# Performance work log

Hardware: AMD Instinct MI355X
Metric: run time of the kernel (lower is better)

Reference implementation:

```python
import jax, jax.numpy as jnp
import numpy as np

B, S, E, H = 4, 1024, 1024, 16
D = E // H
LN_EPS = 1e-5
W_SCALE = 0.02  # keep pre-softmax scores positive and moderate


def _linear(x, W, b):
    return x @ W + b


def _layernorm(x, g, b):
    m = jnp.mean(x, axis=-1, keepdims=True)
    v = jnp.mean((x - m) ** 2, axis=-1, keepdims=True)
    return (x - m) * jax.lax.rsqrt(v + LN_EPS) * g + b


def setup_inputs() -> dict:
    key = jax.random.key(0)
    ks = jax.random.split(key, 24)
    u = lambda k, shape, s=1.0: jax.random.uniform(k, shape, dtype=jnp.float32) * s
    inp = {
        'value': u(ks[0], (B, S, E)),
        'key':   u(ks[1], (B, S, E)),
        'query': u(ks[2], (B, S, E)),
        'mask':  jnp.ones((B, 1, 1, S), dtype=jnp.int32),
        # attention projections (W stored as [in, out])
        'Wv': u(ks[3], (E, E), W_SCALE), 'bv': u(ks[4], (E,), W_SCALE),
        'Wk': u(ks[5], (E, E), W_SCALE), 'bk': u(ks[6], (E,), W_SCALE),
        'Wq': u(ks[7], (E, E), W_SCALE), 'bq': u(ks[8], (E,), W_SCALE),
        'Wo': u(ks[9], (E, E), W_SCALE), 'bo': u(ks[10], (E,), W_SCALE),
        # feed-forward
        'W1': u(ks[11], (E, 4 * E), W_SCALE), 'b1': u(ks[12], (4 * E,), W_SCALE),
        'W2': u(ks[13], (4 * E, E), W_SCALE), 'b2': u(ks[14], (E,), W_SCALE),
        # layer norms
        'g1': jnp.ones((E,), jnp.float32), 'be1': jnp.zeros((E,), jnp.float32),
        'g2': jnp.ones((E,), jnp.float32), 'be2': jnp.zeros((E,), jnp.float32),
    }
    return inp


def reference(value, key, query, mask, Wv, bv, Wk, bk, Wq, bq, Wo, bo,
              W1, b1, W2, b2, g1, be1, g2, be2):
    b, q_len, _ = query.shape
    v = _linear(value, Wv, bv).reshape(b, -1, H, D)   # [B,K,H,D]
    k = _linear(key, Wk, bk).reshape(b, -1, H, D)     # [B,K,H,D]
    q = _linear(query, Wq, bq).reshape(b, q_len, H, D)
    att = jnp.einsum('bqhd,bkhd->bhqk', q, k)         # raw scores
    att = jnp.where(mask == 0, -jnp.inf, att)
    att = jnp.power(att, -0.5)                        # custom score^{-1/2} transform
    att = jax.nn.softmax(att, axis=3)
    ctx = jnp.einsum('bhqk,bkhd->bqhd', att, v).reshape(b, q_len, E)
    attn_out = _linear(ctx, Wo, bo)
    x = _layernorm(attn_out + query, g1, be1)         # dropout = identity (eval)
    ff = _linear(jax.nn.relu(_linear(x, W1, b1)), W2, b2)
    return _layernorm(ff + x, g2, be2)
```

## Files before the change

kernel.cpp:

```cpp
#include <hip/hip_runtime.h>
#include <hip/hip_bf16.h>
#include <cstdint>

typedef __hip_bfloat16 bf16;
typedef float f32x4 __attribute__((ext_vector_type(4)));
typedef short bf16x8 __attribute__((ext_vector_type(8)));
typedef short bf16x4v __attribute__((ext_vector_type(4)));

#define S_LEN 1024
#define EDIM  1024

__device__ __forceinline__ float bfs2f(short s) {
  return __uint_as_float(((unsigned)(unsigned short)s) << 16);
}
__device__ __forceinline__ short f2bfs(float f) {
  union { __hip_bfloat16 h; short s; } u;
  u.h = __float2bfloat16(f);
  return u.s;
}
__device__ __forceinline__ void glds16(const void* g, void* l) {
  __builtin_amdgcn_global_load_lds(
      (const __attribute__((address_space(1))) void*)g,
      (__attribute__((address_space(3))) void*)l, 16, 0, 0);
}
__device__ __forceinline__ float score_xform(float s) {
  float r, e;
  asm("v_rsq_f32 %0, %1" : "=v"(r) : "v"(s));
  r *= 1.44269504088896f;
  asm("v_exp_f32 %0, %1" : "=v"(e) : "v"(r));
  return e;
}
__device__ __forceinline__ int xcd_swz(int bid, int nwg) {
  const int q = nwg >> 3, r = nwg & 7, xcd = bid & 7, j = bid >> 3;
  return (xcd < r ? xcd * (q + 1) : r * (q + 1) + (xcd - r) * q) + j;
}
#define BAR() do { __builtin_amdgcn_s_barrier(); asm volatile("" ::: "memory"); } while (0)
#define WAITV(n) asm volatile("s_waitcnt vmcnt(" #n ")" ::: "memory")

struct Prep { const float* win[6]; bf16* wout[6]; const float* ain[3]; bf16* aout[3]; };
__global__ __launch_bounds__(256)
void k_prep(Prep p) {
  const int t = blockIdx.x;
  const int tid = threadIdx.x;
  if (t < 1536) {
    int z, tr, tc, R, C;
    if (t < 512)       { z = t >> 7;  R = 1024; C = 1024; int i = t & 127;  tr = i >> 4; tc = i & 15; }
    else if (t < 1024) { z = 4; R = 1024; C = 4096; int i = t - 512;  tr = i >> 6; tc = i & 63; }
    else               { z = 5; R = 4096; C = 1024; int i = t - 1024; tr = i >> 4; tc = i & 15; }
    const float* in = p.win[z];
    bf16* out = p.wout[z];
    const int r0 = tr * 128, c0 = tc * 64;
    __shared__ bf16 tlds[64][130];
    const int rr = tid >> 4;
    const int cq = (tid & 15) * 4;
    float4 v[8];
#pragma unroll
    for (int pass = 0; pass < 8; pass++)
      v[pass] = *(const float4*)(in + (size_t)(r0 + pass * 16 + rr) * C + c0 + cq);
#pragma unroll
    for (int pass = 0; pass < 8; pass++) {
      const int r = pass * 16 + rr;
      tlds[cq + 0][r] = __float2bfloat16(v[pass].x);
      tlds[cq + 1][r] = __float2bfloat16(v[pass].y);
      tlds[cq + 2][r] = __float2bfloat16(v[pass].z);
      tlds[cq + 3][r] = __float2bfloat16(v[pass].w);
    }
    __syncthreads();
    const int e8 = (tid & 15) * 8;
    bf16x8 w[4];
#pragma unroll
    for (int pass = 0; pass < 4; pass++)
      w[pass] = *(const bf16x8*)(&tlds[pass * 16 + rr][e8]);
#pragma unroll
    for (int pass = 0; pass < 4; pass++)
      *(bf16x8*)(out + (size_t)(c0 + pass * 16 + rr) * R + r0 + e8) = w[pass];
  } else {
    const int idx = t - 1536;
    const int z = idx >> 8, chunk = idx & 255;
    const float4* in = (const float4*)p.ain[z];
    bf16x4v* out = (bf16x4v*)p.aout[z];
#pragma unroll
    for (int g = 0; g < 2; g++) {
      float4 v[8];
#pragma unroll
      for (int s = 0; s < 8; s++)
        v[s] = in[chunk * 4096 + (g * 8 + s) * 256 + tid];
#pragma unroll
      for (int s = 0; s < 8; s++) {
        bf16x4v o;
        o[0] = f2bfs(v[s].x); o[1] = f2bfs(v[s].y);
        o[2] = f2bfs(v[s].z); o[3] = f2bfs(v[s].w);
        out[chunk * 4096 + (g * 8 + s) * 256 + tid] = o;
      }
    }
  }
}

__global__ void k_transpose_v(const bf16* __restrict__ v, bf16* __restrict__ vt) {
  __shared__ bf16 t[32][33];
  const int bh = blockIdx.z;
  const bf16* in = v + (size_t)(bh >> 4) * S_LEN * EDIM + (bh & 15) * 64;
  bf16* out = vt + (size_t)bh * 64 * S_LEN;
  const int d0 = blockIdx.x * 32, s0 = blockIdx.y * 32;
  const int x = threadIdx.x;
  for (int yy = threadIdx.y; yy < 32; yy += 8)
    t[yy][x] = in[(size_t)(s0 + yy) * EDIM + d0 + x];
  __syncthreads();
  for (int yy = threadIdx.y; yy < 32; yy += 8)
    out[(size_t)(d0 + yy) * S_LEN + s0 + x] = t[x][yy];
}

template <int RELU, int OUT_F32, int HAS_BIAS>
__device__ __forceinline__ void gemm8_body(
    const bf16* __restrict__ A, int lda, const bf16* __restrict__ Bt, int ldb,
    const float* __restrict__ bias, void* __restrict__ Cout, int ldc,
    int K, int koff, int bm, int bn, char* smem) {
  const int tid = threadIdx.x, lane = tid & 63, wid = tid >> 6;
  const int wm = wid >> 2;
  const int wn = wid & 3;
  const int fr = lane & 15, fg = lane >> 4;
  const int sw = (fr & 7) << 4;

  const int rr = lane >> 3;
  const int cc = ((lane & 7) ^ rr) << 3;

  #define STG(src, ld, dstoff)                                                  \
    {                                                                           \
      const bf16* _s = (src);                                                   \
      _Pragma("unroll")                                                         \
      for (int _j = 0; _j < 2; _j++) {                                          \
        const int _L = wid * 2 + _j;                                            \
        glds16(_s + (size_t)(_L * 8 + rr) * (ld) + cc, smem + (dstoff) + _L * 1024); \
      }                                                                         \
    }

  const bf16* Abase = A + (size_t)bm * lda + koff;
  const bf16* Bbase = Bt + (size_t)bn * ldb + koff;
  const int nt = K >> 6;

  STG(Abase, lda, 0);
  STG(Abase + (size_t)128 * lda, lda, 16384);
  STG(Bbase, ldb, 98304);
  STG(Bbase + (size_t)128 * ldb, ldb, 98304 + 16384);
  STG(Abase + 64, lda, 32768);
  STG(Abase + (size_t)128 * lda + 64, lda, 32768 + 16384);
  STG(Bbase + 64, ldb, 131072);
  STG(Bbase + (size_t)128 * ldb + 64, ldb, 131072 + 16384);
  WAITV(8);
  BAR();

  f32x4 acc[8][4] = {};
  bf16x8 af[8][2], bfr[4][2];

  const int aRd = wm * 16384 + fr * 128;
  const int bRd = (wn >> 1) * 16384 + (wn & 1) * 8192 + fr * 128;
  const int c0s = (fg * 16) ^ sw;
  const int c1s = (64 + fg * 16) ^ sw;

  int sa = 0, sb = 0;
  for (int n = 0; n < nt; n++) {
    const char* pa = smem + sa * 32768;
    const char* pb = smem + 98304 + sb * 32768;
    const int kn = (n + 2) << 6;
    const bool st = (n + 2) < nt;
    const int sa2 = (sa >= 1) ? sa - 1 : 2;

#pragma unroll
    for (int j = 0; j < 4; j++) {
      bfr[j][0] = *(const bf16x8*)(pb + bRd + j * 2048 + c0s);
      bfr[j][1] = *(const bf16x8*)(pb + bRd + j * 2048 + c1s);
    }
#pragma unroll
    for (int i = 0; i < 8; i++) {
      af[i][0] = *(const bf16x8*)(pa + aRd + i * 2048 + c0s);
      af[i][1] = *(const bf16x8*)(pa + aRd + i * 2048 + c1s);
    }
    if (st) {
      STG(Abase + kn, lda, sa2 * 32768);
      STG(Abase + (size_t)128 * lda + kn, lda, sa2 * 32768 + 16384);
    }
    BAR();
    __builtin_amdgcn_s_setprio(1);
#pragma unroll
    for (int i = 0; i < 4; i++)
#pragma unroll
      for (int j = 0; j < 4; j++) {
        acc[i][j] = __builtin_amdgcn_mfma_f32_16x16x32_bf16(af[i][0], bfr[j][0], acc[i][j], 0, 0, 0);
        acc[i][j] = __builtin_amdgcn_mfma_f32_16x16x32_bf16(af[i][1], bfr[j][1], acc[i][j], 0, 0, 0);
      }
    __builtin_amdgcn_s_setprio(0);

    if (st) {
      STG(Bbase + kn, ldb, 98304 + sb * 32768);
      STG(Bbase + (size_t)128 * ldb + kn, ldb, 98304 + sb * 32768 + 16384);
    }
    __builtin_amdgcn_s_setprio(1);
#pragma unroll
    for (int i = 0; i < 4; i++)
#pragma unroll
      for (int j = 0; j < 4; j++) {
        acc[i + 4][j] = __builtin_amdgcn_mfma_f32_16x16x32_bf16(af[i + 4][0], bfr[j][0], acc[i + 4][j], 0, 0, 0);
        acc[i + 4][j] = __builtin_amdgcn_mfma_f32_16x16x32_bf16(af[i + 4][1], bfr[j][1], acc[i + 4][j], 0, 0, 0);
      }
    __builtin_amdgcn_s_setprio(0);
    if (st) { WAITV(8); } else { WAITV(0); }
    BAR();
    sa = (sa == 2) ? 0 : sa + 1;
    sb ^= 1;
  }
  #undef STG

  float bv4[4];
#pragma unroll
  for (int j = 0; j < 4; j++)
    bv4[j] = HAS_BIAS ? bias[bn + wn * 64 + j * 16 + fr] : 0.f;
#pragma unroll
  for (int i = 0; i < 8; i++) {
    const size_t rowb = (size_t)bm + wm * 128 + i * 16 + fg * 4;
#pragma unroll
    for (int r = 0; r < 4; r++) {
#pragma unroll
      for (int j = 0; j < 4; j++) {
        float v = acc[i][j][r] + bv4[j];
        if (RELU) v = fmaxf(v, 0.f);
        const size_t idx = (rowb + r) * (size_t)ldc + bn + wn * 64 + j * 16 + fr;
        if (OUT_F32) ((float*)Cout)[idx] = v;
        else ((bf16*)Cout)[idx] = __float2bfloat16(v);
      }
    }
  }
}

struct G8Args {
  const bf16* A; int lda; const bf16* Bt; int ldb; const float* bias;
  void* C[4]; int ldc; int koffz[4]; int Kzz[4];
};
template <int RELU, int OUT_F32, int HAS_BIAS>
__global__ __launch_bounds__(512, 2)
void k_gemm8(G8Args a) {
  __shared__ __align__(16) char smem[163840];
  const int nwg = gridDim.x * gridDim.y;
  const int bid = xcd_swz(blockIdx.y * gridDim.x + blockIdx.x, nwg);
  const int bx = bid % gridDim.x, by = bid / gridDim.x;
  const int z = blockIdx.z;
  gemm8_body<RELU, OUT_F32, HAS_BIAS>(
      a.A, a.lda, a.Bt, a.ldb, a.bias, a.C[z], a.ldc,
      a.Kzz[z], a.koffz[z], by * 256, bx * 256, smem);
}

struct QkvArgs { const bf16* A[3]; const bf16* B[3]; const float* bias[3]; bf16* C[3]; };
__global__ __launch_bounds__(512, 2)
void k_gemm8_qkv(QkvArgs p) {
  __shared__ __align__(16) char smem[163840];
  const int nwg = gridDim.x * gridDim.y;
  const int bid = xcd_swz(blockIdx.y * gridDim.x + blockIdx.x, nwg);
  const int bx = bid % (int)gridDim.x;
  int by = bid / (int)gridDim.x;
  const int grp = by >> 4;
  by &= 15;
  gemm8_body<0, 0, 1>(p.A[grp], 1024, p.B[grp], 1024, p.bias[grp],
                      (void*)p.C[grp], 1024, 1024, 0, by * 256, bx * 256, smem);
}

__global__ __launch_bounds__(256)
void k_attn(const bf16* __restrict__ q, const bf16* __restrict__ k,
            const bf16* __restrict__ vt, bf16* __restrict__ ctx) {
  const int bh = blockIdx.x;
  const int qt = blockIdx.y;
  const int b = bh >> 4, h = bh & 15;
  const int tid = threadIdx.x, lane = tid & 63, w = tid >> 6;
  const int fr = lane & 15, fg = lane >> 4;
  const bf16* Q  = q  + (size_t)b * S_LEN * EDIM + h * 64;
  const bf16* Kp = k  + (size_t)b * S_LEN * EDIM + h * 64;
  const bf16* V  = vt + (size_t)bh * 64 * S_LEN;

  __shared__ __align__(16) bf16 lK[2][64 * 64];
  __shared__ __align__(16) bf16 lV[2][64 * 64];
  __shared__ __align__(16) bf16 eL[4][32][72];

  const int srow = lane >> 3;
  const int scol = (((lane & 7) ^ srow) << 3);
  const int rsw  = (fr & 7) << 3;

  bf16x8 qf[2][2];
#pragma unroll
  for (int i = 0; i < 2; i++)
#pragma unroll
    for (int ks = 0; ks < 2; ks++)
      qf[i][ks] = *(const bf16x8*)(Q + (size_t)(qt * 128 + w * 32 + i * 16 + fr) * EDIM + ks * 32 + fg * 8);

#pragma unroll
  for (int c = 0; c < 2; c++) {
    const int r = w * 8 + c * 32 + srow;
    glds16(Kp + (size_t)r * EDIM + scol, (char*)&lK[0][(w * 8 + c * 32) * 64]);
    glds16(V + (size_t)r * S_LEN + scol, (char*)&lV[0][(w * 8 + c * 32) * 64]);
  }
  __syncthreads();

  f32x4 accO[2][4] = {};
  float lsum[2][4] = {};
  int cur = 0;
  for (int kt = 0; kt < S_LEN; kt += 64) {
    if (kt + 64 < S_LEN) {
#pragma unroll
      for (int c = 0; c < 2; c++) {
        const int r = w * 8 + c * 32 + srow;
        glds16(Kp + (size_t)(kt + 64 + r) * EDIM + scol,
               (char*)&lK[cur ^ 1][(w * 8 + c * 32) * 64]);
        glds16(V + (size_t)r * S_LEN + kt + 64 + scol,
               (char*)&lV[cur ^ 1][(w * 8 + c * 32) * 64]);
      }
    }
    f32x4 accS[2][4] = {};
#pragma unroll
    for (int ks = 0; ks < 2; ks++)
#pragma unroll
      for (int j = 0; j < 4; j++) {
        bf16x8 kf = *(const bf16x8*)(&lK[cur][(j * 16 + fr) * 64 + ((ks * 32 + fg * 8) ^ rsw)]);
#pragma unroll
        for (int i = 0; i < 2; i++)
          accS[i][j] = __builtin_amdgcn_mfma_f32_16x16x32_bf16(qf[i][ks], kf, accS[i][j], 0, 0, 0);
      }
#pragma unroll
    for (int i = 0; i < 2; i++)
#pragma unroll
      for (int j = 0; j < 4; j++)
#pragma unroll
        for (int r = 0; r < 4; r++) {
          float p = score_xform(accS[i][j][r]);
          lsum[i][r] += p;
          eL[w][i * 16 + fg * 4 + r][j * 16 + fr] = __float2bfloat16(p);
        }
#pragma unroll
    for (int ks = 0; ks < 2; ks++) {
      bf16x8 af[2];
#pragma unroll
      for (int i = 0; i < 2; i++)
        af[i] = *(const bf16x8*)(&eL[w][i * 16 + fr][ks * 32 + fg * 8]);
#pragma unroll
      for (int j = 0; j < 4; j++) {
        bf16x8 vf = *(const bf16x8*)(&lV[cur][(j * 16 + fr) * 64 + ((ks * 32 + fg * 8) ^ rsw)]);
#pragma unroll
        for (int i = 0; i < 2; i++)
          accO[i][j] = __builtin_amdgcn_mfma_f32_16x16x32_bf16(af[i], vf, accO[i][j], 0, 0, 0);
      }
    }
    __syncthreads();
    cur ^= 1;
  }

#pragma unroll
  for (int i = 0; i < 2; i++)
#pragma unroll
    for (int r = 0; r < 4; r++) {
      float s = lsum[i][r];
      s += __shfl_xor(s, 1, 64);
      s += __shfl_xor(s, 2, 64);
      s += __shfl_xor(s, 4, 64);
      s += __shfl_xor(s, 8, 64);
      lsum[i][r] = s;
    }
#pragma unroll
  for (int i = 0; i < 2; i++)
#pragma unroll
    for (int r = 0; r < 4; r++) {
      const size_t qrow = (size_t)qt * 128 + w * 32 + i * 16 + fg * 4 + r;
      const float inv = 1.0f / lsum[i][r];
#pragma unroll
      for (int j = 0; j < 4; j++)
        ctx[((size_t)b * S_LEN + qrow) * EDIM + h * 64 + j * 16 + fr] =
            __float2bfloat16(accO[i][j][r] * inv);
    }
}

struct LnP { const void* p[4]; };
template <int NP, int P_BF16, int RES_F32, int OUT_F32>
__global__ __launch_bounds__(256)
void k_ln_resN(LnP pp, const float* __restrict__ bias, const void* res_,
               const float* __restrict__ g, const float* __restrict__ be,
               void* out_) {
  const int row = blockIdx.x;
  const int tid = threadIdx.x;
  const int lane = tid & 63, wid = tid >> 6;
  const size_t base = (size_t)row * EDIM + tid * 4;
  float4 c = *(const float4*)(bias + tid * 4);
  float x[4] = {c.x, c.y, c.z, c.w};
#pragma unroll
  for (int t = 0; t < NP; t++) {
    if (P_BF16) {
      bf16x4v v = *(const bf16x4v*)((const bf16*)pp.p[t] + base);
#pragma unroll
      for (int i = 0; i < 4; i++) x[i] += bfs2f(v[i]);
    } else {
      float4 v = *(const float4*)((const float*)pp.p[t] + base);
      x[0] += v.x; x[1] += v.y; x[2] += v.z; x[3] += v.w;
    }
  }
  if (RES_F32) {
    float4 v = *(const float4*)((const float*)res_ + base);
    x[0] += v.x; x[1] += v.y; x[2] += v.z; x[3] += v.w;
  } else {
    bf16x4v v = *(const bf16x4v*)((const bf16*)res_ + base);
#pragma unroll
    for (int i = 0; i < 4; i++) x[i] += bfs2f(v[i]);
  }

  float s = x[0] + x[1] + x[2] + x[3];
#pragma unroll
  for (int o = 32; o >= 1; o >>= 1) s += __shfl_xor(s, o, 64);
  __shared__ float red[4], red2[4];
  if (lane == 0) red[wid] = s;
  __syncthreads();
  const float mean = (red[0] + red[1] + red[2] + red[3]) * (1.0f / 1024.0f);

  float d[4], s2 = 0.f;
#pragma unroll
  for (int i = 0; i < 4; i++) { d[i] = x[i] - mean; s2 += d[i] * d[i]; }
#pragma unroll
  for (int o = 32; o >= 1; o >>= 1) s2 += __shfl_xor(s2, o, 64);
  if (lane == 0) red2[wid] = s2;
  __syncthreads();
  const float var = (red2[0] + red2[1] + red2[2] + red2[3]) * (1.0f / 1024.0f);
  const float inv = rsqrtf(var + 1e-5f);

  float4 g4 = *(const float4*)(g + tid * 4);
  float4 b4 = *(const float4*)(be + tid * 4);
  float o0 = d[0] * inv * g4.x + b4.x;
  float o1 = d[1] * inv * g4.y + b4.y;
  float o2 = d[2] * inv * g4.z + b4.z;
  float o3 = d[3] * inv * g4.w + b4.w;
  if (OUT_F32) {
    *(float4*)((float*)out_ + base) = make_float4(o0, o1, o2, o3);
  } else {
    bf16x4v o;
    o[0] = f2bfs(o0); o[1] = f2bfs(o1); o[2] = f2bfs(o2); o[3] = f2bfs(o3);
    *(bf16x4v*)((bf16*)out_ + base) = o;
  }
}

extern "C" void kernel_launch(void* const* d_in, const int* in_sizes, int n_in,
                              void* d_out, int out_size, void* d_ws, size_t ws_size,
                              hipStream_t stream) {
  const float* value = (const float*)d_in[0];
  const float* key_  = (const float*)d_in[1];
  const float* query = (const float*)d_in[2];
  const float* Wv = (const float*)d_in[4];  const float* bv = (const float*)d_in[5];
  const float* Wk = (const float*)d_in[6];  const float* bk = (const float*)d_in[7];
  const float* Wq = (const float*)d_in[8];  const float* bq = (const float*)d_in[9];
  const float* Wo = (const float*)d_in[10]; const float* bo = (const float*)d_in[11];
  const float* W1 = (const float*)d_in[12]; const float* b1 = (const float*)d_in[13];
  const float* W2 = (const float*)d_in[14]; const float* b2 = (const float*)d_in[15];
  const float* g1 = (const float*)d_in[16]; const float* be1 = (const float*)d_in[17];
  const float* g2 = (const float*)d_in[18]; const float* be2 = (const float*)d_in[19];

  char* wsb = (char*)d_ws;
  const size_t MB = 1024 * 1024;
  bf16* W1T = (bf16*)(wsb + 0 * MB);
  bf16* W2T = (bf16*)(wsb + 8 * MB);
  bf16* WqT = (bf16*)(wsb + 16 * MB);
  bf16* WkT = (bf16*)(wsb + 18 * MB);
  bf16* WvT = (bf16*)(wsb + 20 * MB);
  bf16* WoT = (bf16*)(wsb + 22 * MB);
  bf16* qx  = (bf16*)(wsb + 24 * MB);
  bf16* kx  = (bf16*)(wsb + 32 * MB);
  bf16* vx  = (bf16*)(wsb + 40 * MB);
  bf16* qb  = (bf16*)(wsb + 48 * MB);
  bf16* kb  = (bf16*)(wsb + 56 * MB);
  bf16* vb  = (bf16*)(wsb + 64 * MB);
  bf16* vtb = (bf16*)(wsb + 72 * MB);
  bf16* ctx = (bf16*)(wsb + 24 * MB);
  float* p0w = (float*)(wsb + 32 * MB);
  float* p1w = (float*)(wsb + 48 * MB);
  float* p2w = (float*)(wsb + 64 * MB);
  bf16* xb  = (bf16*)(wsb + 16 * MB);
  bf16* h1  = (bf16*)(wsb + 24 * MB);
  bf16* fp0 = (bf16*)(wsb + 56 * MB);
  bf16* fp1 = (bf16*)(wsb + 64 * MB);
  bf16* fp2 = (bf16*)(wsb + 72 * MB);
  bf16* fp3 = (bf16*)(wsb + 80 * MB);

  const dim3 tb(32, 8);
  Prep pp;
  pp.win[0] = Wq; pp.wout[0] = WqT;
  pp.win[1] = Wk; pp.wout[1] = WkT;
  pp.win[2] = Wv; pp.wout[2] = WvT;
  pp.win[3] = Wo; pp.wout[3] = WoT;
  pp.win[4] = W1; pp.wout[4] = W1T;
  pp.win[5] = W2; pp.wout[5] = W2T;
  pp.ain[0] = query; pp.aout[0] = qx;
  pp.ain[1] = key_;  pp.aout[1] = kx;
  pp.ain[2] = value; pp.aout[2] = vx;
  k_prep<<<2304, 256, 0, stream>>>(pp);

  QkvArgs qp;
  qp.A[0] = qx; qp.B[0] = WqT; qp.bias[0] = bq; qp.C[0] = qb;
  qp.A[1] = kx; qp.B[1] = WkT; qp.bias[1] = bk; qp.C[1] = kb;
  qp.A[2] = vx; qp.B[2] = WvT; qp.bias[2] = bv; qp.C[2] = vb;
  k_gemm8_qkv<<<dim3(4, 48), 512, 0, stream>>>(qp);

  k_transpose_v<<<dim3(2, 32, 64), tb, 0, stream>>>(vb, vtb);
  k_attn<<<dim3(64, 8), 256, 0, stream>>>(qb, kb, vtb, ctx);

  G8Args wo;
  wo.A = ctx; wo.lda = 1024; wo.Bt = WoT; wo.ldb = 1024; wo.bias = nullptr;
  wo.C[0] = p0w; wo.C[1] = p1w; wo.C[2] = p2w; wo.C[3] = nullptr;
  wo.ldc = 1024;
  wo.koffz[0] = 0;   wo.Kzz[0] = 384;
  wo.koffz[1] = 384; wo.Kzz[1] = 320;
  wo.koffz[2] = 704; wo.Kzz[2] = 320;
  wo.koffz[3] = 0;   wo.Kzz[3] = 64;
  k_gemm8<0, 1, 0><<<dim3(4, 16, 3), 512, 0, stream>>>(wo);
  LnP l1; l1.p[0] = p0w; l1.p[1] = p1w; l1.p[2] = p2w; l1.p[3] = nullptr;
  k_ln_resN<3, 0, 1, 0><<<4096, 256, 0, stream>>>(l1, bo, query, g1, be1, xb);

  G8Args ff1;
  ff1.A = xb; ff1.lda = 1024; ff1.Bt = W1T; ff1.ldb = 1024; ff1.bias = b1;
  ff1.C[0] = h1; ff1.C[1] = nullptr; ff1.C[2] = nullptr; ff1.C[3] = nullptr;
  ff1.ldc = 4096;
  ff1.koffz[0] = 0; ff1.Kzz[0] = 1024;
  ff1.koffz[1] = 0; ff1.Kzz[1] = 64;
  ff1.koffz[2] = 0; ff1.Kzz[2] = 64;
  ff1.koffz[3] = 0; ff1.Kzz[3] = 64;
  k_gemm8<1, 0, 1><<<dim3(16, 16, 1), 512, 0, stream>>>(ff1);

  G8Args ff2;
  ff2.A = h1; ff2.lda = 4096; ff2.Bt = W2T; ff2.ldb = 4096; ff2.bias = nullptr;
  ff2.C[0] = fp0; ff2.C[1] = fp1; ff2.C[2] = fp2; ff2.C[3] = fp3;
  ff2.ldc = 1024;
  for (int z = 0; z < 4; z++) { ff2.koffz[z] = z * 1024; ff2.Kzz[z] = 1024; }
  k_gemm8<0, 0, 0><<<dim3(4, 16, 4), 512, 0, stream>>>(ff2);

  LnP l2;
  l2.p[0] = fp0; l2.p[1] = fp1; l2.p[2] = fp2; l2.p[3] = fp3;
  k_ln_resN<4, 1, 0, 1><<<4096, 256, 0, stream>>>(l2, b2, xb, g2, be2, (float*)d_out);
}
```

Baseline: 213.2 us.

## Fuse fp32-to-bf16 activation conversion into QKV projection GEMM A-loads

```diff
diff --git a/kernel.cpp b/kernel.cpp
--- a/kernel.cpp
+++ b/kernel.cpp
@@ -22,6 +22,12 @@
   __builtin_amdgcn_global_load_lds(
       (const __attribute__((address_space(1))) void*)g,
       (__attribute__((address_space(3))) void*)l, 16, 0, 0);
+}
+__device__ __forceinline__ bf16x8 cvt8(float4 a, float4 b) {
+  bf16x8 w;
+  w[0] = f2bfs(a.x); w[1] = f2bfs(a.y); w[2] = f2bfs(a.z); w[3] = f2bfs(a.w);
+  w[4] = f2bfs(b.x); w[5] = f2bfs(b.y); w[6] = f2bfs(b.z); w[7] = f2bfs(b.w);
+  return w;
 }
 __device__ __forceinline__ float score_xform(float s) {
   float r, e;
@@ -36,64 +42,44 @@
 }
 #define BAR() do { __builtin_amdgcn_s_barrier(); asm volatile("" ::: "memory"); } while (0)
 #define WAITV(n) asm volatile("s_waitcnt vmcnt(" #n ")" ::: "memory")
-
-struct Prep { const float* win[6]; bf16* wout[6]; const float* ain[3]; bf16* aout[3]; };
+#define WAITL0() asm volatile("s_waitcnt lgkmcnt(0)" ::: "memory")
+
+struct Prep { const float* win[6]; bf16* wout[6]; };
 __global__ __launch_bounds__(256)
 void k_prep(Prep p) {
   const int t = blockIdx.x;
   const int tid = threadIdx.x;
-  if (t < 1536) {
-    int z, tr, tc, R, C;
-    if (t < 512)       { z = t >> 7;  R = 1024; C = 1024; int i = t & 127;  tr = i >> 4; tc = i & 15; }
-    else if (t < 1024) { z = 4; R = 1024; C = 4096; int i = t - 512;  tr = i >> 6; tc = i & 63; }
-    else               { z = 5; R = 4096; C = 1024; int i = t - 1024; tr = i >> 4; tc = i & 15; }
-    const float* in = p.win[z];
-    bf16* out = p.wout[z];
-    const int r0 = tr * 128, c0 = tc * 64;
-    __shared__ bf16 tlds[64][130];
-    const int rr = tid >> 4;
-    const int cq = (tid & 15) * 4;
-    float4 v[8];
-#pragma unroll
-    for (int pass = 0; pass < 8; pass++)
-      v[pass] = *(const float4*)(in + (size_t)(r0 + pass * 16 + rr) * C + c0 + cq);
-#pragma unroll
-    for (int pass = 0; pass < 8; pass++) {
-      const int r = pass * 16 + rr;
-      tlds[cq + 0][r] = __float2bfloat16(v[pass].x);
-      tlds[cq + 1][r] = __float2bfloat16(v[pass].y);
-      tlds[cq + 2][r] = __float2bfloat16(v[pass].z);
-      tlds[cq + 3][r] = __float2bfloat16(v[pass].w);
-    }
-    __syncthreads();
-    const int e8 = (tid & 15) * 8;
-    bf16x8 w[4];
-#pragma unroll
-    for (int pass = 0; pass < 4; pass++)
-      w[pass] = *(const bf16x8*)(&tlds[pass * 16 + rr][e8]);
-#pragma unroll
-    for (int pass = 0; pass < 4; pass++)
-      *(bf16x8*)(out + (size_t)(c0 + pass * 16 + rr) * R + r0 + e8) = w[pass];
-  } else {
-    const int idx = t - 1536;
-    const int z = idx >> 8, chunk = idx & 255;
-    const float4* in = (const float4*)p.ain[z];
-    bf16x4v* out = (bf16x4v*)p.aout[z];
-#pragma unroll
-    for (int g = 0; g < 2; g++) {
-      float4 v[8];
-#pragma unroll
-      for (int s = 0; s < 8; s++)
-        v[s] = in[chunk * 4096 + (g * 8 + s) * 256 + tid];
-#pragma unroll
-      for (int s = 0; s < 8; s++) {
-        bf16x4v o;
-        o[0] = f2bfs(v[s].x); o[1] = f2bfs(v[s].y);
-        o[2] = f2bfs(v[s].z); o[3] = f2bfs(v[s].w);
-        out[chunk * 4096 + (g * 8 + s) * 256 + tid] = o;
-      }
-    }
-  }
+  int z, tr, tc, R, C;
+  if (t < 512)       { z = t >> 7;  R = 1024; C = 1024; int i = t & 127;  tr = i >> 4; tc = i & 15; }
+  else if (t < 1024) { z = 4; R = 1024; C = 4096; int i = t - 512;  tr = i >> 6; tc = i & 63; }
+  else               { z = 5; R = 4096; C = 1024; int i = t - 1024; tr = i >> 4; tc = i & 15; }
+  const float* in = p.win[z];
+  bf16* out = p.wout[z];
+  const int r0 = tr * 128, c0 = tc * 64;
+  __shared__ bf16 tlds[64][130];
+  const int rr = tid >> 4;
+  const int cq = (tid & 15) * 4;
+  float4 v[8];
+#pragma unroll
+  for (int pass = 0; pass < 8; pass++)
+    v[pass] = *(const float4*)(in + (size_t)(r0 + pass * 16 + rr) * C + c0 + cq);
+#pragma unroll
+  for (int pass = 0; pass < 8; pass++) {
+    const int r = pass * 16 + rr;
+    tlds[cq + 0][r] = __float2bfloat16(v[pass].x);
+    tlds[cq + 1][r] = __float2bfloat16(v[pass].y);
+    tlds[cq + 2][r] = __float2bfloat16(v[pass].z);
+    tlds[cq + 3][r] = __float2bfloat16(v[pass].w);
+  }
+  __syncthreads();
+  const int e8 = (tid & 15) * 8;
+  bf16x8 w[4];
+#pragma unroll
+  for (int pass = 0; pass < 4; pass++)
+    w[pass] = *(const bf16x8*)(&tlds[pass * 16 + rr][e8]);
+#pragma unroll
+  for (int pass = 0; pass < 4; pass++)
+    *(bf16x8*)(out + (size_t)(c0 + pass * 16 + rr) * R + r0 + e8) = w[pass];
 }
 
 __global__ void k_transpose_v(const bf16* __restrict__ v, bf16* __restrict__ vt) {
@@ -248,9 +234,9 @@
       a.Kzz[z], a.koffz[z], by * 256, bx * 256, smem);
 }
 
-struct QkvArgs { const bf16* A[3]; const bf16* B[3]; const float* bias[3]; bf16* C[3]; };
+struct QkvfArgs { const float* A[3]; const bf16* B[3]; const float* bias[3]; bf16* C[3]; };
 __global__ __launch_bounds__(512, 2)
-void k_gemm8_qkv(QkvArgs p) {
+void k_gemm8_qkvf(QkvfArgs p) {
   __shared__ __align__(16) char smem[163840];
   const int nwg = gridDim.x * gridDim.y;
   const int bid = xcd_swz(blockIdx.y * gridDim.x + blockIdx.x, nwg);
@@ -258,8 +244,148 @@
   int by = bid / (int)gridDim.x;
   const int grp = by >> 4;
   by &= 15;
-  gemm8_body<0, 0, 1>(p.A[grp], 1024, p.B[grp], 1024, p.bias[grp],
-                      (void*)p.C[grp], 1024, 1024, 0, by * 256, bx * 256, smem);
+  const float* A = p.A[grp];
+  const bf16* Bt = p.B[grp];
+  const float* bias = p.bias[grp];
+  bf16* Cout = p.C[grp];
+  const int bm = by * 256, bn = bx * 256;
+
+  const int tid = threadIdx.x, lane = tid & 63, wid = tid >> 6;
+  const int wm = wid >> 2, wn = wid & 3;
+  const int fr = lane & 15, fg = lane >> 4;
+  const int sw = (fr & 7) << 4;
+  const int rr = lane >> 3;
+  const int cc = ((lane & 7) ^ rr) << 3;
+
+  int aRow[4], aCol[4], aByte[4];
+#pragma unroll
+  for (int s = 0; s < 4; s++) {
+    const int cidx = tid + s * 512;
+    const int m = cidx >> 3, c = cidx & 7;
+    aRow[s] = m;
+    aCol[s] = (c ^ (m & 7)) * 8;
+    aByte[s] = cidx * 16;
+  }
+  const float* Af = A + (size_t)bm * 1024;
+
+  #define STGB(src, dstoff)                                                     \
+    {                                                                           \
+      const bf16* _s = (src);                                                   \
+      _Pragma("unroll")                                                         \
+      for (int _j = 0; _j < 2; _j++) {                                          \
+        const int _L = wid * 2 + _j;                                            \
+        glds16(_s + (size_t)(_L * 8 + rr) * 1024 + cc, smem + (dstoff) + _L * 1024); \
+      }                                                                         \
+    }
+
+  const bf16* Bbase = Bt + (size_t)bn * 1024;
+  float4 va[8];
+
+  STGB(Bbase, 65536);
+  STGB(Bbase + (size_t)128 * 1024, 65536 + 16384);
+  STGB(Bbase + 64, 98304);
+  STGB(Bbase + (size_t)128 * 1024 + 64, 98304 + 16384);
+#pragma unroll
+  for (int s = 0; s < 4; s++) {
+    va[2 * s]     = *(const float4*)(Af + (size_t)aRow[s] * 1024 + aCol[s]);
+    va[2 * s + 1] = *(const float4*)(Af + (size_t)aRow[s] * 1024 + aCol[s] + 4);
+  }
+  WAITV(0);
+#pragma unroll
+  for (int s = 0; s < 4; s++)
+    *(bf16x8*)(smem + aByte[s]) = cvt8(va[2 * s], va[2 * s + 1]);
+  WAITL0();
+  BAR();
+
+  f32x4 acc[8][4] = {};
+  bf16x8 af[8][2], bfr[4][2];
+  const int aRd = wm * 16384 + fr * 128;
+  const int bRd = (wn >> 1) * 16384 + (wn & 1) * 8192 + fr * 128;
+  const int c0s = (fg * 16) ^ sw;
+  const int c1s = (64 + fg * 16) ^ sw;
+  const int nt = 16;
+
+  int sb = 0;
+  for (int n = 0; n < nt; n++) {
+    const char* pa = smem + (n & 1) * 32768;
+    const char* pb = smem + 65536 + sb * 32768;
+    const bool stA = (n + 1) < nt;
+    const bool stB = (n + 2) < nt;
+
+#pragma unroll
+    for (int j = 0; j < 4; j++) {
+      bfr[j][0] = *(const bf16x8*)(pb + bRd + j * 2048 + c0s);
+      bfr[j][1] = *(const bf16x8*)(pb + bRd + j * 2048 + c1s);
+    }
+#pragma unroll
+    for (int i = 0; i < 8; i++) {
+      af[i][0] = *(const bf16x8*)(pa + aRd + i * 2048 + c0s);
+      af[i][1] = *(const bf16x8*)(pa + aRd + i * 2048 + c1s);
+    }
+    if (stA) {
+      const int kofs = (n + 1) << 6;
+#pragma unroll
+      for (int s = 0; s < 4; s++) {
+        va[2 * s]     = *(const float4*)(Af + (size_t)aRow[s] * 1024 + kofs + aCol[s]);
+        va[2 * s + 1] = *(const float4*)(Af + (size_t)aRow[s] * 1024 + kofs + aCol[s] + 4);
+      }
+    }
+    BAR();
+    __builtin_amdgcn_s_setprio(1);
+#pragma unroll
+    for (int i = 0; i < 4; i++)
+#pragma unroll
+      for (int j = 0; j < 4; j++) {
+        acc[i][j] = __builtin_amdgcn_mfma_f32_16x16x32_bf16(af[i][0], bfr[j][0], acc[i][j], 0, 0, 0);
+        acc[i][j] = __builtin_amdgcn_mfma_f32_16x16x32_bf16(af[i][1], bfr[j][1], acc[i][j], 0, 0, 0);
+      }
+    __builtin_amdgcn_s_setprio(0);
+
+    if (stB) {
+      const int kB = (n + 2) << 6;
+      const int dst = 65536 + ((sb + 2) % 3) * 32768;
+      STGB(Bbase + kB, dst);
+      STGB(Bbase + (size_t)128 * 1024 + kB, dst + 16384);
+    }
+    if (stA) {
+      if (stB) { WAITV(4); } else { WAITV(0); }
+      char* wd = smem + ((n + 1) & 1) * 32768;
+#pragma unroll
+      for (int s = 0; s < 4; s++)
+        *(bf16x8*)(wd + aByte[s]) = cvt8(va[2 * s], va[2 * s + 1]);
+    }
+    __builtin_amdgcn_s_setprio(1);
+#pragma unroll
+    for (int i = 0; i < 4; i++)
+#pragma unroll
+      for (int j = 0; j < 4; j++) {
+        acc[i + 4][j] = __builtin_amdgcn_mfma_f32_16x16x32_bf16(af[i + 4][0], bfr[j][0], acc[i + 4][j], 0, 0, 0);
+        acc[i + 4][j] = __builtin_amdgcn_mfma_f32_16x16x32_bf16(af[i + 4][1], bfr[j][1], acc[i + 4][j], 0, 0, 0);
+      }
+    __builtin_amdgcn_s_setprio(0);
+    WAITL0();
+    BAR();
+    sb = (sb == 2) ? 0 : sb + 1;
+  }
+  #undef STGB
+
+  float bv4[4];
+#pragma unroll
+  for (int j = 0; j < 4; j++)
+    bv4[j] = bias[bn + wn * 64 + j * 16 + fr];
+#pragma unroll
+  for (int i = 0; i < 8; i++) {
+    const size_t rowb = (size_t)bm + wm * 128 + i * 16 + fg * 4;
+#pragma unroll
+    for (int r = 0; r < 4; r++) {
+#pragma unroll
+      for (int j = 0; j < 4; j++) {
+        float v = acc[i][j][r] + bv4[j];
+        const size_t idx = (rowb + r) * (size_t)1024 + bn + wn * 64 + j * 16 + fr;
+        Cout[idx] = __float2bfloat16(v);
+      }
+    }
+  }
 }
 
 __global__ __launch_bounds__(256)
@@ -461,9 +587,6 @@
   bf16* WkT = (bf16*)(wsb + 18 * MB);
   bf16* WvT = (bf16*)(wsb + 20 * MB);
   bf16* WoT = (bf16*)(wsb + 22 * MB);
-  bf16* qx  = (bf16*)(wsb + 24 * MB);
-  bf16* kx  = (bf16*)(wsb + 32 * MB);
-  bf16* vx  = (bf16*)(wsb + 40 * MB);
   bf16* qb  = (bf16*)(wsb + 48 * MB);
   bf16* kb  = (bf16*)(wsb + 56 * MB);
   bf16* vb  = (bf16*)(wsb + 64 * MB);
@@ -487,16 +610,13 @@
   pp.win[3] = Wo; pp.wout[3] = WoT;
   pp.win[4] = W1; pp.wout[4] = W1T;
   pp.win[5] = W2; pp.wout[5] = W2T;
-  pp.ain[0] = query; pp.aout[0] = qx;
-  pp.ain[1] = key_;  pp.aout[1] = kx;
-  pp.ain[2] = value; pp.aout[2] = vx;
-  k_prep<<<2304, 256, 0, stream>>>(pp);
-
-  QkvArgs qp;
-  qp.A[0] = qx; qp.B[0] = WqT; qp.bias[0] = bq; qp.C[0] = qb;
-  qp.A[1] = kx; qp.B[1] = WkT; qp.bias[1] = bk; qp.C[1] = kb;
-  qp.A[2] = vx; qp.B[2] = WvT; qp.bias[2] = bv; qp.C[2] = vb;
-  k_gemm8_qkv<<<dim3(4, 48), 512, 0, stream>>>(qp);
+  k_prep<<<1536, 256, 0, stream>>>(pp);
+
+  QkvfArgs qp;
+  qp.A[0] = query; qp.B[0] = WqT; qp.bias[0] = bq; qp.C[0] = qb;
+  qp.A[1] = key_;  qp.B[1] = WkT; qp.bias[1] = bk; qp.C[1] = kb;
+  qp.A[2] = value; qp.B[2] = WvT; qp.bias[2] = bv; qp.C[2] = vb;
+  k_gemm8_qkvf<<<dim3(4, 48), 512, 0, stream>>>(qp);
 
   k_transpose_v<<<dim3(2, 32, 64), tb, 0, stream>>>(vb, vtb);
   k_attn<<<dim3(64, 8), 256, 0, stream>>>(qb, kb, vtb, ctx);
```

Result: slower. 252.9 us (+18.6%).
